# Kernel tuning notes

Hardware: AMD Instinct MI355X
Metric: run time of the kernel (lower is better)

## Reference

```python
import jax, jax.numpy as jnp
import numpy as np

SCALING = 16.0 / 16.0  # lora_alpha / r

def setup_inputs() -> dict:
    key = jax.random.key(0)
    k1, k2, k3, k4, k5 = jax.random.split(key, 5)
    B, S, D, R = 4, 4096, 4096, 16
    x = jax.random.normal(k1, (B, S, D), dtype=jnp.float32)
    W = jax.random.normal(k2, (D, D), dtype=jnp.float32) * (1.0 / np.sqrt(D))
    bias = jax.random.normal(k3, (D,), dtype=jnp.float32) * 0.02
    lora_A = jax.random.normal(k4, (D, R), dtype=jnp.float32) * (1.0 / np.sqrt(D))
    lora_B = jax.random.normal(k5, (R, D), dtype=jnp.float32) * 0.02
    return {"x": x, "W": W, "bias": bias, "lora_A": lora_A, "lora_B": lora_B}

def reference(x, W, bias, lora_A, lora_B):
    x_dtype = x.dtype
    # base (quantized) linear modeled as dense GEMM: [B,S,D] @ [D,D]
    out = jnp.einsum('bsd,df->bsf', x, W)
    # low-rank LoRA path: (x @ A) @ B * scaling, computed in train_dtype then cast back
    lora = jnp.einsum('bsr,rf->bsf', jnp.einsum('bsd,dr->bsr', x.astype(lora_A.dtype), lora_A), lora_B) * SCALING
    out = out + lora.astype(x_dtype)
    out = out + bias.astype(x_dtype)
    return out
```

## Files before the change

kernel.cpp:

```cpp
#include <hip/hip_runtime.h>
#include <hip/hip_bf16.h>


typedef __attribute__((ext_vector_type(8))) __bf16 bf16x8;
typedef __attribute__((ext_vector_type(4))) float f32x4;

#define M_DIM 16384
#define N_DIM 4096
#define K_DIM 4096

__device__ __forceinline__ void async16(const void* g, void* l) {
    __builtin_amdgcn_global_load_lds((const __attribute__((address_space(1))) void*)g,
                                     (__attribute__((address_space(3))) void*)l,
                                     16, 0, 0);
}

__global__ void cast_x_kernel(const float* __restrict__ x, __bf16* __restrict__ xb, size_t n) {
    size_t i0 = ((size_t)blockIdx.x * blockDim.x + threadIdx.x) * 8;
    size_t stride = (size_t)gridDim.x * blockDim.x * 8;
    for (size_t i = i0; i < n; i += stride) {
        f32x4 v0 = __builtin_nontemporal_load((const f32x4*)(x + i));
        f32x4 v1 = __builtin_nontemporal_load((const f32x4*)(x + i + 4));
        bf16x8 o;
        o[0] = (__bf16)v0[0]; o[1] = (__bf16)v0[1]; o[2] = (__bf16)v0[2]; o[3] = (__bf16)v0[3];
        o[4] = (__bf16)v1[0]; o[5] = (__bf16)v1[1]; o[6] = (__bf16)v1[2]; o[7] = (__bf16)v1[3];
        *(bf16x8*)(xb + i) = o;
    }
}

__global__ void prep_w_kernel(const float* __restrict__ W, const float* __restrict__ A,
                              const float* __restrict__ Bm, __bf16* __restrict__ Wt) {
    __shared__ float Ws[32][33];
    __shared__ float As[32][16];
    __shared__ float Bs[16][32];
    const int tx = threadIdx.x;
    const int ty = threadIdx.y;
    const int t = ty * 32 + tx;
    const int n0 = blockIdx.x * 32;
    const int k0 = blockIdx.y * 32;

#pragma unroll
    for (int i = 0; i < 4; ++i) {
        int k = ty + i * 8;
        Ws[k][tx] = W[(size_t)(k0 + k) * N_DIM + n0 + tx];
    }
    for (int i = t; i < 512; i += 256)
        As[i >> 4][i & 15] = A[(size_t)(k0 + (i >> 4)) * 16 + (i & 15)];
    for (int i = t; i < 512; i += 256)
        Bs[i >> 5][i & 31] = Bm[(size_t)(i >> 5) * N_DIM + n0 + (i & 31)];
    __syncthreads();

    float a[16];
#pragma unroll
    for (int r = 0; r < 16; ++r) a[r] = As[tx][r];
#pragma unroll
    for (int i = 0; i < 4; ++i) {
        int n = ty + i * 8;
        float acc = Ws[tx][n];
#pragma unroll
        for (int r = 0; r < 16; ++r) acc += a[r] * Bs[r][n];
        Wt[(size_t)(n0 + n) * K_DIM + k0 + tx] = (__bf16)acc;
    }
}


#define WAIT_VM(N) asm volatile("s_waitcnt vmcnt(" #N ")" ::: "memory")
#define BARRIER() do { asm volatile("" ::: "memory"); __builtin_amdgcn_s_barrier(); asm volatile("" ::: "memory"); } while (0)

#define STAGE_A(ldsbase, row0, kt) do {                                              \
    int r_ = (row0) + srow;                                                          \
    async16(Xb + (size_t)(m0 + r_) * K_DIM + (kt) + scol,                            \
            (ldsbase) + (row0) * 128 + sldsoff); } while (0)

#define STAGE_B(ldsbase, row0, kt) do {                                              \
    int p_ = (row0) + srow;                                                          \
    int nl_ = ((p_ >> 5) & 3) * 64 + ((p_ >> 7) & 1) * 32 + (p_ & 31);               \
    async16(Wt + (size_t)(n0 + nl_) * K_DIM + (kt) + scol,                           \
            (ldsbase) + (row0) * 128 + sldsoff); } while (0)

#define LOAD_AF(ldsbase, MH)                                                         \
    _Pragma("unroll") for (int m_ = 0; m_ < 4; ++m_)                                 \
    _Pragma("unroll") for (int ks_ = 0; ks_ < 2; ++ks_)                              \
        afr[m_][ks_] = *(const bf16x8*)((ldsbase) + aRowB + (MH) * 8192 + m_ * 2048 + colsw[ks_]);

#define LOAD_BF(dst, ldsbase, NH)                                                    \
    _Pragma("unroll") for (int n_ = 0; n_ < 2; ++n_)                                 \
    _Pragma("unroll") for (int ks_ = 0; ks_ < 2; ++ks_)                              \
        dst[n_][ks_] = *(const bf16x8*)((ldsbase) + bRowB + (NH) * 16384 + n_ * 2048 + colsw[ks_]);

#define MFMA_Q(MH, NH, BF)                                                           \
    __builtin_amdgcn_s_setprio(1);                                                   \
    _Pragma("unroll") for (int m_ = 0; m_ < 4; ++m_)                                 \
    _Pragma("unroll") for (int n_ = 0; n_ < 2; ++n_)                                 \
    _Pragma("unroll") for (int ks_ = 0; ks_ < 2; ++ks_)                              \
        acc[(MH) * 4 + m_][(NH) * 2 + n_] = __builtin_amdgcn_mfma_f32_16x16x32_bf16( \
            afr[m_][ks_], BF[n_][ks_], acc[(MH) * 4 + m_][(NH) * 2 + n_], 0, 0, 0);  \
    __builtin_amdgcn_s_setprio(0);                                                   \
    __builtin_amdgcn_sched_barrier(0);

#define TILE_FULL(AC, BC, AO, BO, KT)                                                \
    LOAD_AF(AC, 0); LOAD_BF(b0f, BC, 0);                                             \
    STAGE_B(BO, 0, (KT) + 64); STAGE_B(BO, 64, (KT) + 64);                           \
    BARRIER(); MFMA_Q(0, 0, b0f); BARRIER();                                         \
    LOAD_BF(b1f, BC, 1);                                                             \
    STAGE_A(AO, 64, (KT) + 64); STAGE_A(AO, 192, (KT) + 64);                         \
    BARRIER(); MFMA_Q(0, 1, b1f); WAIT_VM(8); BARRIER();                             \
    LOAD_AF(AC, 1);                                                                  \
    STAGE_A(AC, 0, (KT) + 128); STAGE_A(AC, 128, (KT) + 128);                        \
    BARRIER(); MFMA_Q(1, 1, b1f); BARRIER();                                         \
    STAGE_B(BC, 128, (KT) + 128); STAGE_B(BC, 192, (KT) + 128);                      \
    BARRIER(); MFMA_Q(1, 0, b0f); WAIT_VM(6); BARRIER();

__global__ __launch_bounds__(512, 2) void gemm256_kernel(
    const __bf16* __restrict__ Xb, const __bf16* __restrict__ Wt,
    const float* __restrict__ bias, float* __restrict__ out) {
    extern __shared__ __align__(16) char smem[];
    const int tid  = threadIdx.x;
    const int lane = tid & 63;
    const int wave = tid >> 6;
    const int wr = wave >> 2;
    const int wn = wave & 3;

    const int bid = blockIdx.x;
    const int wg = (bid & 7) * 128 + (bid >> 3);
    const int m0 = (wg >> 4) * 256;
    const int n0 = (wg & 15) * 256;

    char* A0 = smem;
    char* B0 = smem + 32768;
    char* A1 = smem + 65536;
    char* B1 = smem + 98304;

    const int srow = tid >> 3;
    const int scol = ((tid & 7) ^ (srow & 7)) << 3;
    const int sldsoff = wave * 1024;

    int colsw[2];
#pragma unroll
    for (int ks = 0; ks < 2; ++ks)
        colsw[ks] = ((ks * 32 + (lane >> 4) * 8) ^ ((lane & 7) * 8)) << 1;
    const int aRowB = (wr * 128 + (lane & 15)) * 128;
    const int bRowB = (wn * 32 + (lane & 15)) * 128;

    f32x4 acc[8][4] = {};
    bf16x8 afr[4][2], b0f[2][2], b1f[2][2];

    STAGE_A(A0, 0, 0);    STAGE_A(A0, 128, 0);
    STAGE_B(B0, 0, 0);    STAGE_B(B0, 64, 0);
    STAGE_A(A0, 64, 0);   STAGE_A(A0, 192, 0);
    STAGE_B(B0, 128, 0);  STAGE_B(B0, 192, 0);
    STAGE_A(A1, 0, 64);   STAGE_A(A1, 128, 64);
    STAGE_B(B1, 128, 64); STAGE_B(B1, 192, 64);
    WAIT_VM(4);
    BARRIER();

    for (int it = 0; it < 31; ++it) {
        const int kt = it * 128;
        TILE_FULL(A0, B0, A1, B1, kt);
        TILE_FULL(A1, B1, A0, B0, kt + 64);
    }

    LOAD_AF(A0, 0); LOAD_BF(b0f, B0, 0);
    STAGE_B(B1, 0, 4032); STAGE_B(B1, 64, 4032);
    BARRIER(); MFMA_Q(0, 0, b0f); BARRIER();
    LOAD_BF(b1f, B0, 1);
    STAGE_A(A1, 64, 4032); STAGE_A(A1, 192, 4032);
    BARRIER(); MFMA_Q(0, 1, b1f); WAIT_VM(8); BARRIER();
    LOAD_AF(A0, 1);
    BARRIER(); MFMA_Q(1, 1, b1f); BARRIER();
    BARRIER(); MFMA_Q(1, 0, b0f); WAIT_VM(2); BARRIER();

    LOAD_AF(A1, 0); LOAD_BF(b0f, B1, 0);
    BARRIER(); MFMA_Q(0, 0, b0f); BARRIER();
    LOAD_BF(b1f, B1, 1);
    BARRIER(); MFMA_Q(0, 1, b1f); WAIT_VM(0); BARRIER();
    LOAD_AF(A1, 1);
    BARRIER(); MFMA_Q(1, 1, b1f); BARRIER();
    MFMA_Q(1, 0, b0f);

#pragma unroll
    for (int mh = 0; mh < 2; ++mh)
#pragma unroll
        for (int m = 0; m < 4; ++m) {
            const int gr = m0 + wr * 128 + mh * 64 + m * 16 + (lane >> 4) * 4;
#pragma unroll
            for (int nh = 0; nh < 2; ++nh)
#pragma unroll
                for (int n = 0; n < 2; ++n) {
                    const int gc = n0 + wn * 64 + nh * 32 + n * 16 + (lane & 15);
                    const float bv = bias[gc];
                    const f32x4 a = acc[mh * 4 + m][nh * 2 + n];
#pragma unroll
                    for (int j = 0; j < 4; ++j)
                        __builtin_nontemporal_store(a[j] + bv,
                            &out[(size_t)(gr + j) * N_DIM + gc]);
                }
        }
}

extern "C" void kernel_launch(void* const* d_in, const int* in_sizes, int n_in,
                              void* d_out, int out_size, void* d_ws, size_t ws_size,
                              hipStream_t stream) {
    const float* x    = (const float*)d_in[0];
    const float* W    = (const float*)d_in[1];
    const float* bias = (const float*)d_in[2];
    const float* lA   = (const float*)d_in[3];
    const float* lB   = (const float*)d_in[4];
    float* out = (float*)d_out;

    __bf16* Xb = (__bf16*)d_ws;
    __bf16* Wt = (__bf16*)((char*)d_ws + (size_t)M_DIM * K_DIM * 2);

    cast_x_kernel<<<2048, 256, 0, stream>>>(x, Xb, (size_t)M_DIM * K_DIM);
    prep_w_kernel<<<dim3(N_DIM / 32, K_DIM / 32), dim3(32, 8), 0, stream>>>(W, lA, lB, Wt);

    (void)hipFuncSetAttribute((const void*)gemm256_kernel,
                              hipFuncAttributeMaxDynamicSharedMemorySize, 131072);
    gemm256_kernel<<<1024, 512, 131072, stream>>>(Xb, Wt, bias, out);
}
```

Baseline: 576.7 us.

## Switch GEMM to 32x32x16 MFMA and restructure LDS staging schedule

Replaces the 16x16x32 bf16 MFMA tiles with 32x32x16 MFMA, so each wave computes 4x2 32x32 accumulators and reads fewer LDS fragments per FLOP. The per-tile pipeline becomes two phases, each issuing the whole next-stage A or B tile, with new swizzled column offsets and a rewritten prologue, tail and epilogue store mapping. This aims to cut LDS read traffic and instruction overhead per MFMA. The risks are higher register pressure from the larger accumulator and fragment arrays, and a new wait-count schedule that must match the new load ordering.

```diff
diff --git a/kernel.cpp b/kernel.cpp
--- a/kernel.cpp
+++ b/kernel.cpp
@@ -4,6 +4,7 @@
 
 typedef __attribute__((ext_vector_type(8))) __bf16 bf16x8;
 typedef __attribute__((ext_vector_type(4))) float f32x4;
+typedef __attribute__((ext_vector_type(16))) float f32x16;
 
 #define M_DIM 16384
 #define N_DIM 4096
@@ -78,38 +79,41 @@
     async16(Wt + (size_t)(n0 + nl_) * K_DIM + (kt) + scol,                           \
             (ldsbase) + (row0) * 128 + sldsoff); } while (0)
 
-#define LOAD_AF(ldsbase, MH)                                                         \
-    _Pragma("unroll") for (int m_ = 0; m_ < 4; ++m_)                                 \
-    _Pragma("unroll") for (int ks_ = 0; ks_ < 2; ++ks_)                              \
-        afr[m_][ks_] = *(const bf16x8*)((ldsbase) + aRowB + (MH) * 8192 + m_ * 2048 + colsw[ks_]);
-
-#define LOAD_BF(dst, ldsbase, NH)                                                    \
-    _Pragma("unroll") for (int n_ = 0; n_ < 2; ++n_)                                 \
-    _Pragma("unroll") for (int ks_ = 0; ks_ < 2; ++ks_)                              \
-        dst[n_][ks_] = *(const bf16x8*)((ldsbase) + bRowB + (NH) * 16384 + n_ * 2048 + colsw[ks_]);
-
-#define MFMA_Q(MH, NH, BF)                                                           \
+#define DS_A(buf, MTG, KC) (*(const bf16x8*)((buf) + aRow32 + (MTG) * 4096 + colswk[KC]))
+#define DS_B(buf, NT, KC)  (*(const bf16x8*)((buf) + bRow32 + (NT) * 16384 + colswk[KC]))
+
+#define P0_CORE(AC, BC)                                                              \
+    _Pragma("unroll") for (int mt_ = 0; mt_ < 2; ++mt_)                              \
+    _Pragma("unroll") for (int kc_ = 0; kc_ < 4; ++kc_)                              \
+        afr[mt_][kc_] = DS_A(AC, mt_, kc_);                                          \
+    _Pragma("unroll") for (int nt_ = 0; nt_ < 2; ++nt_)                              \
+    _Pragma("unroll") for (int kc_ = 0; kc_ < 4; ++kc_)                              \
+        bfr[nt_][kc_] = DS_B(BC, nt_, kc_);
+
+#define P1_CORE(AC)                                                                  \
+    _Pragma("unroll") for (int mt_ = 0; mt_ < 2; ++mt_)                              \
+    _Pragma("unroll") for (int kc_ = 0; kc_ < 4; ++kc_)                              \
+        afr[mt_][kc_] = DS_A(AC, 2 + mt_, kc_);
+
+#define MFMA16(MBASE)                                                                \
     __builtin_amdgcn_s_setprio(1);                                                   \
-    _Pragma("unroll") for (int m_ = 0; m_ < 4; ++m_)                                 \
-    _Pragma("unroll") for (int n_ = 0; n_ < 2; ++n_)                                 \
-    _Pragma("unroll") for (int ks_ = 0; ks_ < 2; ++ks_)                              \
-        acc[(MH) * 4 + m_][(NH) * 2 + n_] = __builtin_amdgcn_mfma_f32_16x16x32_bf16( \
-            afr[m_][ks_], BF[n_][ks_], acc[(MH) * 4 + m_][(NH) * 2 + n_], 0, 0, 0);  \
+    _Pragma("unroll") for (int kc_ = 0; kc_ < 4; ++kc_)                              \
+    _Pragma("unroll") for (int mt_ = 0; mt_ < 2; ++mt_)                              \
+    _Pragma("unroll") for (int nt_ = 0; nt_ < 2; ++nt_)                              \
+        acc[(MBASE) + mt_][nt_] = __builtin_amdgcn_mfma_f32_32x32x16_bf16(           \
+            afr[mt_][kc_], bfr[nt_][kc_], acc[(MBASE) + mt_][nt_], 0, 0, 0);         \
     __builtin_amdgcn_s_setprio(0);                                                   \
     __builtin_amdgcn_sched_barrier(0);
 
-#define TILE_FULL(AC, BC, AO, BO, KT)                                                \
-    LOAD_AF(AC, 0); LOAD_BF(b0f, BC, 0);                                             \
-    STAGE_B(BO, 0, (KT) + 64); STAGE_B(BO, 64, (KT) + 64);                           \
-    BARRIER(); MFMA_Q(0, 0, b0f); BARRIER();                                         \
-    LOAD_BF(b1f, BC, 1);                                                             \
+#define TILE2(AC, BC, AO, KT)                                                        \
+    P0_CORE(AC, BC);                                                                 \
+    STAGE_A(AO, 0, (KT) + 64);  STAGE_A(AO, 128, (KT) + 64);                         \
     STAGE_A(AO, 64, (KT) + 64); STAGE_A(AO, 192, (KT) + 64);                         \
-    BARRIER(); MFMA_Q(0, 1, b1f); WAIT_VM(8); BARRIER();                             \
-    LOAD_AF(AC, 1);                                                                  \
-    STAGE_A(AC, 0, (KT) + 128); STAGE_A(AC, 128, (KT) + 128);                        \
-    BARRIER(); MFMA_Q(1, 1, b1f); BARRIER();                                         \
+    BARRIER(); MFMA16(0); WAIT_VM(8); BARRIER();                                     \
+    P1_CORE(AC);                                                                     \
+    STAGE_B(BC, 0, (KT) + 128);  STAGE_B(BC, 64, (KT) + 128);                        \
     STAGE_B(BC, 128, (KT) + 128); STAGE_B(BC, 192, (KT) + 128);                      \
-    BARRIER(); MFMA_Q(1, 0, b0f); WAIT_VM(6); BARRIER();
+    BARRIER(); MFMA16(2); WAIT_VM(6); BARRIER();
 
 __global__ __launch_bounds__(512, 2) void gemm256_kernel(
     const __bf16* __restrict__ Xb, const __bf16* __restrict__ Wt,
@@ -135,67 +139,56 @@
     const int scol = ((tid & 7) ^ (srow & 7)) << 3;
     const int sldsoff = wave * 1024;
 
-    int colsw[2];
-#pragma unroll
-    for (int ks = 0; ks < 2; ++ks)
-        colsw[ks] = ((ks * 32 + (lane >> 4) * 8) ^ ((lane & 7) * 8)) << 1;
-    const int aRowB = (wr * 128 + (lane & 15)) * 128;
-    const int bRowB = (wn * 32 + (lane & 15)) * 128;
-
-    f32x4 acc[8][4] = {};
-    bf16x8 afr[4][2], b0f[2][2], b1f[2][2];
-
-    STAGE_A(A0, 0, 0);    STAGE_A(A0, 128, 0);
-    STAGE_B(B0, 0, 0);    STAGE_B(B0, 64, 0);
-    STAGE_A(A0, 64, 0);   STAGE_A(A0, 192, 0);
-    STAGE_B(B0, 128, 0);  STAGE_B(B0, 192, 0);
-    STAGE_A(A1, 0, 64);   STAGE_A(A1, 128, 64);
-    STAGE_B(B1, 128, 64); STAGE_B(B1, 192, 64);
-    WAIT_VM(4);
+    int colswk[4];
+#pragma unroll
+    for (int kc = 0; kc < 4; ++kc)
+        colswk[kc] = ((kc * 16 + (lane >> 5) * 8) << 1) ^ ((lane & 7) << 4);
+    const int aRow32 = (wr * 128 + (lane & 31)) * 128;
+    const int bRow32 = (wn * 32 + (lane & 31)) * 128;
+
+    f32x16 acc[4][2] = {};
+    bf16x8 afr[2][4], bfr[2][4];
+
+    STAGE_B(B0, 0, 0);   STAGE_B(B0, 64, 0);  STAGE_B(B0, 128, 0); STAGE_B(B0, 192, 0);
+    STAGE_A(A0, 0, 0);   STAGE_A(A0, 128, 0);
+    STAGE_A(A0, 64, 0);  STAGE_A(A0, 192, 0);
+    STAGE_B(B1, 0, 64);  STAGE_B(B1, 64, 64); STAGE_B(B1, 128, 64); STAGE_B(B1, 192, 64);
+    WAIT_VM(6);
     BARRIER();
 
     for (int it = 0; it < 31; ++it) {
         const int kt = it * 128;
-        TILE_FULL(A0, B0, A1, B1, kt);
-        TILE_FULL(A1, B1, A0, B0, kt + 64);
-    }
-
-    LOAD_AF(A0, 0); LOAD_BF(b0f, B0, 0);
-    STAGE_B(B1, 0, 4032); STAGE_B(B1, 64, 4032);
-    BARRIER(); MFMA_Q(0, 0, b0f); BARRIER();
-    LOAD_BF(b1f, B0, 1);
+        TILE2(A0, B0, A1, kt);
+        TILE2(A1, B1, A0, kt + 64);
+    }
+
+    P0_CORE(A0, B0);
+    STAGE_A(A1, 0, 4032);  STAGE_A(A1, 128, 4032);
     STAGE_A(A1, 64, 4032); STAGE_A(A1, 192, 4032);
-    BARRIER(); MFMA_Q(0, 1, b1f); WAIT_VM(8); BARRIER();
-    LOAD_AF(A0, 1);
-    BARRIER(); MFMA_Q(1, 1, b1f); BARRIER();
-    BARRIER(); MFMA_Q(1, 0, b0f); WAIT_VM(2); BARRIER();
-
-    LOAD_AF(A1, 0); LOAD_BF(b0f, B1, 0);
-    BARRIER(); MFMA_Q(0, 0, b0f); BARRIER();
-    LOAD_BF(b1f, B1, 1);
-    BARRIER(); MFMA_Q(0, 1, b1f); WAIT_VM(0); BARRIER();
-    LOAD_AF(A1, 1);
-    BARRIER(); MFMA_Q(1, 1, b1f); BARRIER();
-    MFMA_Q(1, 0, b0f);
-
-#pragma unroll
-    for (int mh = 0; mh < 2; ++mh)
-#pragma unroll
-        for (int m = 0; m < 4; ++m) {
-            const int gr = m0 + wr * 128 + mh * 64 + m * 16 + (lane >> 4) * 4;
-#pragma unroll
-            for (int nh = 0; nh < 2; ++nh)
-#pragma unroll
-                for (int n = 0; n < 2; ++n) {
-                    const int gc = n0 + wn * 64 + nh * 32 + n * 16 + (lane & 15);
-                    const float bv = bias[gc];
-                    const f32x4 a = acc[mh * 4 + m][nh * 2 + n];
-#pragma unroll
-                    for (int j = 0; j < 4; ++j)
-                        __builtin_nontemporal_store(a[j] + bv,
-                            &out[(size_t)(gr + j) * N_DIM + gc]);
-                }
+    BARRIER(); MFMA16(0); WAIT_VM(8); BARRIER();
+    P1_CORE(A0);
+    BARRIER(); MFMA16(2); WAIT_VM(2); BARRIER();
+
+    P0_CORE(A1, B1);
+    BARRIER(); MFMA16(0); WAIT_VM(0); BARRIER();
+    P1_CORE(A1);
+    BARRIER(); MFMA16(2);
+
+#pragma unroll
+    for (int mtG = 0; mtG < 4; ++mtG) {
+#pragma unroll
+        for (int nt = 0; nt < 2; ++nt) {
+            const int gc = n0 + wn * 64 + nt * 32 + (lane & 31);
+            const float bv = bias[gc];
+            const f32x16 a = acc[mtG][nt];
+#pragma unroll
+            for (int j = 0; j < 16; ++j) {
+                const int row = (j & 3) + 8 * (j >> 2) + 4 * (lane >> 5);
+                const int gr = m0 + wr * 128 + mtG * 32 + row;
+                __builtin_nontemporal_store(a[j] + bv, &out[(size_t)gr * N_DIM + gc]);
+            }
         }
+    }
 }
 
 extern "C" void kernel_launch(void* const* d_in, const int* in_sizes, int n_in,
```

Result: slower. 646.6 us (+12.1%).

## Load B fragments directly from global memory into registers, halving LDS usage

Applied to the files above, without the earlier changes.

The W (B operand) tile no longer goes through LDS. Each wave now loads its own B fragments straight from global memory into registers, one K-step ahead. Only A stays double-buffered in LDS, so shared memory drops from 128KB to 64KB and the per-step schedule is simplified into two phases. The aim is to cut LDS traffic and staging overhead. The cost is redundant global/L2 reads of B, since the two wave rows in a block each load the same B fragments, plus longer global-latency exposure on the MFMA critical path.

```diff
diff --git a/kernel.cpp b/kernel.cpp
--- a/kernel.cpp
+++ b/kernel.cpp
@@ -72,44 +72,36 @@
     async16(Xb + (size_t)(m0 + r_) * K_DIM + (kt) + scol,                            \
             (ldsbase) + (row0) * 128 + sldsoff); } while (0)
 
-#define STAGE_B(ldsbase, row0, kt) do {                                              \
-    int p_ = (row0) + srow;                                                          \
-    int nl_ = ((p_ >> 5) & 3) * 64 + ((p_ >> 7) & 1) * 32 + (p_ & 31);               \
-    async16(Wt + (size_t)(n0 + nl_) * K_DIM + (kt) + scol,                           \
-            (ldsbase) + (row0) * 128 + sldsoff); } while (0)
-
 #define LOAD_AF(ldsbase, MH)                                                         \
     _Pragma("unroll") for (int m_ = 0; m_ < 4; ++m_)                                 \
     _Pragma("unroll") for (int ks_ = 0; ks_ < 2; ++ks_)                              \
         afr[m_][ks_] = *(const bf16x8*)((ldsbase) + aRowB + (MH) * 8192 + m_ * 2048 + colsw[ks_]);
 
-#define LOAD_BF(dst, ldsbase, NH)                                                    \
-    _Pragma("unroll") for (int n_ = 0; n_ < 2; ++n_)                                 \
+#define BLOAD(KT2)                                                                   \
+    _Pragma("unroll") for (int nh_ = 0; nh_ < 2; ++nh_)                              \
+    _Pragma("unroll") for (int nf_ = 0; nf_ < 2; ++nf_)                              \
     _Pragma("unroll") for (int ks_ = 0; ks_ < 2; ++ks_)                              \
-        dst[n_][ks_] = *(const bf16x8*)((ldsbase) + bRowB + (NH) * 16384 + n_ * 2048 + colsw[ks_]);
-
-#define MFMA_Q(MH, NH, BF)                                                           \
+        bfr[nh_][nf_][ks_] = *(const bf16x8*)(bbase[nh_][nf_] + (KT2) + ks_ * 32);
+
+#define MFMA32(MH)                                                                   \
     __builtin_amdgcn_s_setprio(1);                                                   \
+    _Pragma("unroll") for (int ks_ = 0; ks_ < 2; ++ks_)                              \
     _Pragma("unroll") for (int m_ = 0; m_ < 4; ++m_)                                 \
-    _Pragma("unroll") for (int n_ = 0; n_ < 2; ++n_)                                 \
-    _Pragma("unroll") for (int ks_ = 0; ks_ < 2; ++ks_)                              \
-        acc[(MH) * 4 + m_][(NH) * 2 + n_] = __builtin_amdgcn_mfma_f32_16x16x32_bf16( \
-            afr[m_][ks_], BF[n_][ks_], acc[(MH) * 4 + m_][(NH) * 2 + n_], 0, 0, 0);  \
-    __builtin_amdgcn_s_setprio(0);                                                   \
-    __builtin_amdgcn_sched_barrier(0);
-
-#define TILE_FULL(AC, BC, AO, BO, KT)                                                \
-    LOAD_AF(AC, 0); LOAD_BF(b0f, BC, 0);                                             \
-    STAGE_B(BO, 0, (KT) + 64); STAGE_B(BO, 64, (KT) + 64);                           \
-    BARRIER(); MFMA_Q(0, 0, b0f); BARRIER();                                         \
-    LOAD_BF(b1f, BC, 1);                                                             \
+    _Pragma("unroll") for (int nh_ = 0; nh_ < 2; ++nh_)                              \
+    _Pragma("unroll") for (int nf_ = 0; nf_ < 2; ++nf_)                              \
+        acc[(MH) * 4 + m_][nh_ * 2 + nf_] = __builtin_amdgcn_mfma_f32_16x16x32_bf16( \
+            afr[m_][ks_], bfr[nh_][nf_][ks_], acc[(MH) * 4 + m_][nh_ * 2 + nf_], 0, 0, 0); \
+    __builtin_amdgcn_s_setprio(0);
+
+#define PH0(AC, AO, KT)                                                              \
+    LOAD_AF(AC, 0);                                                                  \
+    STAGE_A(AO, 0, (KT) + 64); STAGE_A(AO, 128, (KT) + 64);                          \
+    BARRIER(); MFMA32(0); WAIT_VM(2); BARRIER();
+
+#define PH1(AC, AO, KT)                                                              \
+    LOAD_AF(AC, 1);                                                                  \
     STAGE_A(AO, 64, (KT) + 64); STAGE_A(AO, 192, (KT) + 64);                         \
-    BARRIER(); MFMA_Q(0, 1, b1f); WAIT_VM(8); BARRIER();                             \
-    LOAD_AF(AC, 1);                                                                  \
-    STAGE_A(AC, 0, (KT) + 128); STAGE_A(AC, 128, (KT) + 128);                        \
-    BARRIER(); MFMA_Q(1, 1, b1f); BARRIER();                                         \
-    STAGE_B(BC, 128, (KT) + 128); STAGE_B(BC, 192, (KT) + 128);                      \
-    BARRIER(); MFMA_Q(1, 0, b0f); WAIT_VM(6); BARRIER();
+    BARRIER(); MFMA32(1); BLOAD((KT) + 64); WAIT_VM(10); BARRIER();
 
 __global__ __launch_bounds__(512, 2) void gemm256_kernel(
     const __bf16* __restrict__ Xb, const __bf16* __restrict__ Wt,
@@ -127,9 +119,7 @@
     const int n0 = (wg & 15) * 256;
 
     char* A0 = smem;
-    char* B0 = smem + 32768;
-    char* A1 = smem + 65536;
-    char* B1 = smem + 98304;
+    char* A1 = smem + 32768;
 
     const int srow = tid >> 3;
     const int scol = ((tid & 7) ^ (srow & 7)) << 3;
@@ -140,43 +130,37 @@
     for (int ks = 0; ks < 2; ++ks)
         colsw[ks] = ((ks * 32 + (lane >> 4) * 8) ^ ((lane & 7) * 8)) << 1;
     const int aRowB = (wr * 128 + (lane & 15)) * 128;
-    const int bRowB = (wn * 32 + (lane & 15)) * 128;
+
+    const __bf16* bbase[2][2];
+#pragma unroll
+    for (int nh = 0; nh < 2; ++nh)
+#pragma unroll
+        for (int nf = 0; nf < 2; ++nf)
+            bbase[nh][nf] = Wt + (size_t)(n0 + wn * 64 + nh * 32 + nf * 16 + (lane & 15)) * K_DIM
+                               + (lane >> 4) * 8;
 
     f32x4 acc[8][4] = {};
-    bf16x8 afr[4][2], b0f[2][2], b1f[2][2];
-
-    STAGE_A(A0, 0, 0);    STAGE_A(A0, 128, 0);
-    STAGE_B(B0, 0, 0);    STAGE_B(B0, 64, 0);
-    STAGE_A(A0, 64, 0);   STAGE_A(A0, 192, 0);
-    STAGE_B(B0, 128, 0);  STAGE_B(B0, 192, 0);
-    STAGE_A(A1, 0, 64);   STAGE_A(A1, 128, 64);
-    STAGE_B(B1, 128, 64); STAGE_B(B1, 192, 64);
-    WAIT_VM(4);
+    bf16x8 afr[4][2], bfr[2][2][2];
+
+    STAGE_A(A0, 0, 0);  STAGE_A(A0, 128, 0);
+    BLOAD(0);
+    STAGE_A(A0, 64, 0); STAGE_A(A0, 192, 0);
+    WAIT_VM(10);
     BARRIER();
 
     for (int it = 0; it < 31; ++it) {
         const int kt = it * 128;
-        TILE_FULL(A0, B0, A1, B1, kt);
-        TILE_FULL(A1, B1, A0, B0, kt + 64);
-    }
-
-    LOAD_AF(A0, 0); LOAD_BF(b0f, B0, 0);
-    STAGE_B(B1, 0, 4032); STAGE_B(B1, 64, 4032);
-    BARRIER(); MFMA_Q(0, 0, b0f); BARRIER();
-    LOAD_BF(b1f, B0, 1);
-    STAGE_A(A1, 64, 4032); STAGE_A(A1, 192, 4032);
-    BARRIER(); MFMA_Q(0, 1, b1f); WAIT_VM(8); BARRIER();
-    LOAD_AF(A0, 1);
-    BARRIER(); MFMA_Q(1, 1, b1f); BARRIER();
-    BARRIER(); MFMA_Q(1, 0, b0f); WAIT_VM(2); BARRIER();
-
-    LOAD_AF(A1, 0); LOAD_BF(b0f, B1, 0);
-    BARRIER(); MFMA_Q(0, 0, b0f); BARRIER();
-    LOAD_BF(b1f, B1, 1);
-    BARRIER(); MFMA_Q(0, 1, b1f); WAIT_VM(0); BARRIER();
+        PH0(A0, A1, kt);       PH1(A0, A1, kt);
+        PH0(A1, A0, kt + 64);  PH1(A1, A0, kt + 64);
+    }
+
+    PH0(A0, A1, 3968);
+    PH1(A0, A1, 3968);
+
+    LOAD_AF(A1, 0);
+    BARRIER(); MFMA32(0); WAIT_VM(0); BARRIER();
     LOAD_AF(A1, 1);
-    BARRIER(); MFMA_Q(1, 1, b1f); BARRIER();
-    MFMA_Q(1, 0, b0f);
+    BARRIER(); MFMA32(1);
 
 #pragma unroll
     for (int mh = 0; mh < 2; ++mh)
@@ -215,6 +199,6 @@
     prep_w_kernel<<<dim3(N_DIM / 32, K_DIM / 32), dim3(32, 8), 0, stream>>>(W, lA, lB, Wt);
 
     (void)hipFuncSetAttribute((const void*)gemm256_kernel,
-                              hipFuncAttributeMaxDynamicSharedMemorySize, 131072);
-    gemm256_kernel<<<1024, 512, 131072, stream>>>(Xb, Wt, bias, out);
-}
+                              hipFuncAttributeMaxDynamicSharedMemorySize, 65536);
+    gemm256_kernel<<<1024, 512, 65536, stream>>>(Xb, Wt, bias, out);
+}
```

Result: slower. 882.8 us (+53.1%).

## Restructure GEMM main loop into two 32-MFMA phases with fewer barriers

Applied to the files above, without the earlier changes.

Replaces the four-quadrant MFMA schedule per K tile with two phases of 32 MFMAs each. All B fragments are loaded up front, and A and B tiles are staged as whole blocks per phase instead of being interleaved across quadrants. This halves the number of barriers per tile and changes the prefetch order and wait counts. The trade-off is higher register pressure and coarser overlap of global-to-LDS loads with compute, and the reworked wait counts could expose more load latency.

```diff
diff --git a/kernel.cpp b/kernel.cpp
--- a/kernel.cpp
+++ b/kernel.cpp
@@ -88,28 +88,32 @@
     _Pragma("unroll") for (int ks_ = 0; ks_ < 2; ++ks_)                              \
         dst[n_][ks_] = *(const bf16x8*)((ldsbase) + bRowB + (NH) * 16384 + n_ * 2048 + colsw[ks_]);
 
-#define MFMA_Q(MH, NH, BF)                                                           \
+#define MFMA32(MH)                                                                   \
     __builtin_amdgcn_s_setprio(1);                                                   \
-    _Pragma("unroll") for (int m_ = 0; m_ < 4; ++m_)                                 \
-    _Pragma("unroll") for (int n_ = 0; n_ < 2; ++n_)                                 \
     _Pragma("unroll") for (int ks_ = 0; ks_ < 2; ++ks_)                              \
-        acc[(MH) * 4 + m_][(NH) * 2 + n_] = __builtin_amdgcn_mfma_f32_16x16x32_bf16( \
-            afr[m_][ks_], BF[n_][ks_], acc[(MH) * 4 + m_][(NH) * 2 + n_], 0, 0, 0);  \
+    _Pragma("unroll") for (int m_ = 0; m_ < 4; ++m_) {                               \
+        _Pragma("unroll") for (int n_ = 0; n_ < 2; ++n_)                             \
+            acc[(MH) * 4 + m_][n_] = __builtin_amdgcn_mfma_f32_16x16x32_bf16(        \
+                afr[m_][ks_], b0f[n_][ks_], acc[(MH) * 4 + m_][n_], 0, 0, 0);        \
+        _Pragma("unroll") for (int n_ = 0; n_ < 2; ++n_)                             \
+            acc[(MH) * 4 + m_][2 + n_] = __builtin_amdgcn_mfma_f32_16x16x32_bf16(    \
+                afr[m_][ks_], b1f[n_][ks_], acc[(MH) * 4 + m_][2 + n_], 0, 0, 0);    \
+    }                                                                                \
     __builtin_amdgcn_s_setprio(0);                                                   \
     __builtin_amdgcn_sched_barrier(0);
 
-#define TILE_FULL(AC, BC, AO, BO, KT)                                                \
-    LOAD_AF(AC, 0); LOAD_BF(b0f, BC, 0);                                             \
-    STAGE_B(BO, 0, (KT) + 64); STAGE_B(BO, 64, (KT) + 64);                           \
-    BARRIER(); MFMA_Q(0, 0, b0f); BARRIER();                                         \
-    LOAD_BF(b1f, BC, 1);                                                             \
+#define PH0(AC, BC, AO, KT)                                                          \
+    LOAD_AF(AC, 0);                                                                  \
+    LOAD_BF(b0f, BC, 0); LOAD_BF(b1f, BC, 1);                                        \
+    STAGE_A(AO, 0, (KT) + 64);  STAGE_A(AO, 128, (KT) + 64);                         \
     STAGE_A(AO, 64, (KT) + 64); STAGE_A(AO, 192, (KT) + 64);                         \
-    BARRIER(); MFMA_Q(0, 1, b1f); WAIT_VM(8); BARRIER();                             \
+    BARRIER(); MFMA32(0); BARRIER();
+
+#define PH1(AC, BC, KT)                                                              \
     LOAD_AF(AC, 1);                                                                  \
-    STAGE_A(AC, 0, (KT) + 128); STAGE_A(AC, 128, (KT) + 128);                        \
-    BARRIER(); MFMA_Q(1, 1, b1f); BARRIER();                                         \
+    STAGE_B(BC, 0, (KT) + 128);   STAGE_B(BC, 64, (KT) + 128);                       \
     STAGE_B(BC, 128, (KT) + 128); STAGE_B(BC, 192, (KT) + 128);                      \
-    BARRIER(); MFMA_Q(1, 0, b0f); WAIT_VM(6); BARRIER();
+    BARRIER(); MFMA32(1); WAIT_VM(4); BARRIER();
 
 __global__ __launch_bounds__(512, 2) void gemm256_kernel(
     const __bf16* __restrict__ Xb, const __bf16* __restrict__ Wt,
@@ -145,38 +149,27 @@
     f32x4 acc[8][4] = {};
     bf16x8 afr[4][2], b0f[2][2], b1f[2][2];
 
-    STAGE_A(A0, 0, 0);    STAGE_A(A0, 128, 0);
-    STAGE_B(B0, 0, 0);    STAGE_B(B0, 64, 0);
-    STAGE_A(A0, 64, 0);   STAGE_A(A0, 192, 0);
-    STAGE_B(B0, 128, 0);  STAGE_B(B0, 192, 0);
-    STAGE_A(A1, 0, 64);   STAGE_A(A1, 128, 64);
-    STAGE_B(B1, 128, 64); STAGE_B(B1, 192, 64);
+    STAGE_B(B0, 0, 0);   STAGE_B(B0, 64, 0);  STAGE_B(B0, 128, 0); STAGE_B(B0, 192, 0);
+    STAGE_A(A0, 0, 0);   STAGE_A(A0, 128, 0); STAGE_A(A0, 64, 0);  STAGE_A(A0, 192, 0);
+    STAGE_B(B1, 0, 64);  STAGE_B(B1, 64, 64); STAGE_B(B1, 128, 64); STAGE_B(B1, 192, 64);
     WAIT_VM(4);
     BARRIER();
 
     for (int it = 0; it < 31; ++it) {
         const int kt = it * 128;
-        TILE_FULL(A0, B0, A1, B1, kt);
-        TILE_FULL(A1, B1, A0, B0, kt + 64);
-    }
-
-    LOAD_AF(A0, 0); LOAD_BF(b0f, B0, 0);
-    STAGE_B(B1, 0, 4032); STAGE_B(B1, 64, 4032);
-    BARRIER(); MFMA_Q(0, 0, b0f); BARRIER();
-    LOAD_BF(b1f, B0, 1);
-    STAGE_A(A1, 64, 4032); STAGE_A(A1, 192, 4032);
-    BARRIER(); MFMA_Q(0, 1, b1f); WAIT_VM(8); BARRIER();
+        PH0(A0, B0, A1, kt);       PH1(A0, B0, kt);
+        PH0(A1, B1, A0, kt + 64);  PH1(A1, B1, kt + 64);
+    }
+
+    PH0(A0, B0, A1, 3968);
     LOAD_AF(A0, 1);
-    BARRIER(); MFMA_Q(1, 1, b1f); BARRIER();
-    BARRIER(); MFMA_Q(1, 0, b0f); WAIT_VM(2); BARRIER();
-
-    LOAD_AF(A1, 0); LOAD_BF(b0f, B1, 0);
-    BARRIER(); MFMA_Q(0, 0, b0f); BARRIER();
-    LOAD_BF(b1f, B1, 1);
-    BARRIER(); MFMA_Q(0, 1, b1f); WAIT_VM(0); BARRIER();
+    BARRIER(); MFMA32(1); WAIT_VM(0); BARRIER();
+
+    LOAD_AF(A1, 0);
+    LOAD_BF(b0f, B1, 0); LOAD_BF(b1f, B1, 1);
+    BARRIER(); MFMA32(0); BARRIER();
     LOAD_AF(A1, 1);
-    BARRIER(); MFMA_Q(1, 1, b1f); BARRIER();
-    MFMA_Q(1, 0, b0f);
+    MFMA32(1);
 
 #pragma unroll
     for (int mh = 0; mh < 2; ++mh)
```

Result: no change. 587.6 us (+1.9%).
